# Performance work log

Measured on AMD Instinct MI355X. Metric: run time of the kernel, lower is better.

The kernel has to match this reference:

```python
import jax, jax.numpy as jnp
import numpy as np

K = 10          # top-k history news selected per candidate
THRESHOLD = 0.1 # attention-weight threshold (config.threshold)
EPS = 1e-12     # F.normalize eps


def setup_inputs() -> dict:
    key = jax.random.key(0)
    k1, k2, k3, k4 = jax.random.split(key, 4)
    B, C, H, L, LEV, D = 32, 5, 50, 32, 3, 256
    return {
        "cdd_repr": jax.random.normal(k1, (B, C, D), dtype=jnp.float32),
        "his_repr": jax.random.normal(k2, (B, H, D), dtype=jnp.float32),
        "his_embedding": jax.random.normal(k3, (B, H, L, LEV, D), dtype=jnp.float32),
        "W_sel": jax.random.normal(k4, (D, D), dtype=jnp.float32) * (1.0 / np.sqrt(D)),
        "b_sel": jnp.zeros((D,), dtype=jnp.float32),
    }


def _l2norm(x):
    # F.normalize(x, dim=-1): x / max(||x||, eps)
    n = jnp.sqrt(jnp.sum(x * x, axis=-1, keepdims=True))
    return x / jnp.maximum(n, EPS)


def reference(cdd_repr, his_repr, his_embedding, W_sel, b_sel):
    # selectionProject (Linear) + L2 normalize
    c = _l2norm(cdd_repr @ W_sel + b_sel)      # [B, C, D]
    h = _l2norm(his_repr @ W_sel + b_sel)      # [B, H, D]
    # news-level attention scores: cdd x his
    attn = jnp.einsum('bcd,bhd->bch', c, h)    # [B, C, H]
    # top-k over history
    w, idx = jax.lax.top_k(attn, K)            # [B, C, K]
    # gather selected history embeddings: [B, C, K, L, LEV, D]
    B = his_embedding.shape[0]
    his_activated = his_embedding[jnp.arange(B)[:, None, None], idx]
    # threshold masking then scale activated embeddings by attention weight
    w_masked = jnp.where(w < THRESHOLD, 0.0, w)
    his_activated = his_activated * w_masked[:, :, :, None, None, None]
    return his_activated
```

## Files before the change

kernel.cpp:

```cpp
#include <hip/hip_runtime.h>
#include <math.h>

#define BB 32
#define CC 5
#define HH 50
#define LL 32
#define LEV 3
#define DD 256
#define KK 10
#define THRESH 0.1f
#define EPSF 1e-12f
#define RPB 4
#define NPROJ ((BB * CC + BB * HH) / RPB)
#define INNER (LL * LEV * DD)
#define INNER4 (INNER / 4)
#define CHUNKS 4
#define PERCH (INNER4 / CHUNKS)

typedef float f32x4 __attribute__((ext_vector_type(4)));

__global__ void proj_norm_kernel(const float* __restrict__ cdd,
                                 const float* __restrict__ his,
                                 const float* __restrict__ W,
                                 const float* __restrict__ bias,
                                 float* __restrict__ c_out,
                                 float* __restrict__ h_out)
{
    const int row0 = blockIdx.x * RPB;
    const int j    = threadIdx.x;
    const int wid  = j >> 6;
    const int lane = j & 63;

    __shared__ float xs[RPB][DD];
    #pragma unroll
    for (int r = 0; r < RPB; ++r) {
        const int row = row0 + r;
        const float* x = (row < BB * CC) ? (cdd + (size_t)row * DD)
                                         : (his + (size_t)(row - BB * CC) * DD);
        xs[r][j] = x[j];
    }
    __syncthreads();

    const float bj = bias[j];
    float acc[RPB];
    #pragma unroll
    for (int r = 0; r < RPB; ++r) acc[r] = bj;

    for (int d = 0; d < DD; d += 4) {
        const float w0 = W[(size_t)(d + 0) * DD + j];
        const float w1 = W[(size_t)(d + 1) * DD + j];
        const float w2 = W[(size_t)(d + 2) * DD + j];
        const float w3 = W[(size_t)(d + 3) * DD + j];
        #pragma unroll
        for (int r = 0; r < RPB; ++r) {
            const float4 xv = *(const float4*)&xs[r][d];
            acc[r] = fmaf(xv.x, w0, fmaf(xv.y, w1, fmaf(xv.z, w2, fmaf(xv.w, w3, acc[r]))));
        }
    }

    __shared__ float part[RPB][4];
    #pragma unroll
    for (int r = 0; r < RPB; ++r) {
        float s = acc[r] * acc[r];
        #pragma unroll
        for (int off = 32; off > 0; off >>= 1) s += __shfl_xor(s, off, 64);
        if (lane == 0) part[r][wid] = s;
    }
    __syncthreads();
    __shared__ float inv_s[RPB];
    if (j < RPB) {
        const float s = part[j][0] + part[j][1] + part[j][2] + part[j][3];
        inv_s[j] = 1.0f / fmaxf(sqrtf(s), EPSF);
    }
    __syncthreads();

    #pragma unroll
    for (int r = 0; r < RPB; ++r) {
        const int row = row0 + r;
        float* y = (row < BB * CC) ? (c_out + (size_t)row * DD)
                                   : (h_out + (size_t)(row - BB * CC) * DD);
        y[j] = acc[r] * inv_s[r];
    }
}

__global__ void attn_topk_kernel(const float* __restrict__ c_n,
                                 const float* __restrict__ h_n,
                                 float2* __restrict__ wvidx)
{
    const int bc   = blockIdx.x;
    const int b    = bc / CC;
    const int tid  = threadIdx.x;
    const int wid  = tid >> 6;
    const int lane = tid & 63;

    __shared__ float cs[DD];
    __shared__ float attn_s[64];
    cs[tid] = c_n[(size_t)bc * DD + tid];
    if (tid < 64) attn_s[tid] = -INFINITY;
    __syncthreads();

    for (int h = wid; h < HH; h += 4) {
        const float* hr = h_n + (size_t)(b * HH + h) * DD;
        float p = 0.f;
        #pragma unroll
        for (int i = 0; i < 4; ++i) p += cs[lane + i * 64] * hr[lane + i * 64];
        #pragma unroll
        for (int off = 32; off > 0; off >>= 1) p += __shfl_down(p, off, 64);
        if (lane == 0) attn_s[h] = p;
    }
    __syncthreads();

    if (wid == 0) {
        float v   = attn_s[lane];
        int   myi = lane;
        for (int k = 0; k < KK; ++k) {
            float bv = v;
            int   bi = myi;
            #pragma unroll
            for (int off = 32; off > 0; off >>= 1) {
                const float ov = __shfl_xor(bv, off, 64);
                const int   oi = __shfl_xor(bi, off, 64);
                if (ov > bv || (ov == bv && oi < bi)) { bv = ov; bi = oi; }
            }
            if (lane == 0)
                wvidx[bc * KK + k] = make_float2((bv < THRESH) ? 0.0f : bv,
                                                 __int_as_float(bi));
            if (myi == bi) v = -INFINITY;
        }
    }
}

__global__ __launch_bounds__(256)
void gather_scale_kernel(const float* __restrict__ emb,
                         const float2* __restrict__ wvidx,
                         float* __restrict__ out)
{
    const int g     = blockIdx.x;
    const int blk   = g >> 2;
    const int chunk = g & 3;
    const int b     = blk / (CC * KK);

    const float2 wi = wvidx[blk];
    const float  w_ = wi.x;

    f32x4* dst = (f32x4*)(out + (size_t)blk * INNER) + chunk * PERCH + threadIdx.x;

    if (w_ == 0.0f) {
        const f32x4 z = (f32x4){0.f, 0.f, 0.f, 0.f};
        #pragma unroll
        for (int u = 0; u < PERCH / 256; ++u)
            __builtin_nontemporal_store(z, dst + 256 * u);
    } else {
        const int hi = __float_as_int(wi.y);
        const f32x4* src = (const f32x4*)(emb + (size_t)(b * HH + hi) * INNER)
                           + chunk * PERCH + threadIdx.x;
        f32x4 v[PERCH / 256];
        #pragma unroll
        for (int u = 0; u < PERCH / 256; ++u)
            v[u] = src[256 * u];
        #pragma unroll
        for (int u = 0; u < PERCH / 256; ++u)
            __builtin_nontemporal_store(v[u] * w_, dst + 256 * u);
    }
}

extern "C" void kernel_launch(void* const* d_in, const int* in_sizes, int n_in,
                              void* d_out, int out_size, void* d_ws, size_t ws_size,
                              hipStream_t stream) {
    const float* cdd  = (const float*)d_in[0];
    const float* his  = (const float*)d_in[1];
    const float* emb  = (const float*)d_in[2];
    const float* W    = (const float*)d_in[3];
    const float* bias = (const float*)d_in[4];
    float* out = (float*)d_out;

    char* ws = (char*)d_ws;
    float*  c_n   = (float*)ws;
    float*  h_n   = (float*)(ws + 163840);
    float2* wvidx = (float2*)(ws + 163840 + 1638400);

    proj_norm_kernel<<<NPROJ, DD, 0, stream>>>(cdd, his, W, bias, c_n, h_n);
    attn_topk_kernel<<<BB * CC, DD, 0, stream>>>(c_n, h_n, wvidx);
    gather_scale_kernel<<<BB * CC * KK * CHUNKS, 256, 0, stream>>>(emb, wvidx, out);
}
```

Measured before the change: 93.34 us.

## Replace per-row gather blocks with grid-stride flat gather and double projection rows

The gather/scale kernel becomes a persistent grid-stride loop over the whole flattened output with a fixed 2048 blocks. Each block first copies the full weight/index table into shared memory. Each element is then processed with a per-element index division and a branch, instead of a fixed 4-chunk block per selected row. The projection kernel now handles 8 rows per block instead of 4, which halves how often W is re-read. In exchange, each element pays an integer divide and each block loads the 1600-entry table, and each thread now has only one load in flight per iteration instead of several unrolled ones.

```diff
diff --git a/kernel.cpp b/kernel.cpp
--- a/kernel.cpp
+++ b/kernel.cpp
@@ -10,12 +10,13 @@
 #define KK 10
 #define THRESH 0.1f
 #define EPSF 1e-12f
-#define RPB 4
+#define RPB 8
 #define NPROJ ((BB * CC + BB * HH) / RPB)
 #define INNER (LL * LEV * DD)
 #define INNER4 (INNER / 4)
-#define CHUNKS 4
-#define PERCH (INNER4 / CHUNKS)
+#define NBCK (BB * CC * KK)
+#define TOTAL4 (NBCK * INNER4)
+#define NGBLK 2048
 
 typedef float f32x4 __attribute__((ext_vector_type(4)));
 
@@ -131,36 +132,32 @@
 }
 
 __global__ __launch_bounds__(256)
-void gather_scale_kernel(const float* __restrict__ emb,
-                         const float2* __restrict__ wvidx,
-                         float* __restrict__ out)
+void gather_flat_kernel(const float* __restrict__ emb,
+                        const float2* __restrict__ wvidx,
+                        float* __restrict__ out)
 {
-    const int g     = blockIdx.x;
-    const int blk   = g >> 2;
-    const int chunk = g & 3;
-    const int b     = blk / (CC * KK);
+    __shared__ float2 tbl[NBCK];
+    for (int t = threadIdx.x; t < NBCK; t += 256)
+        tbl[t] = wvidx[t];
+    __syncthreads();
 
-    const float2 wi = wvidx[blk];
-    const float  w_ = wi.x;
+    const f32x4* __restrict__ src4 = (const f32x4*)emb;
+    f32x4* __restrict__ dst4       = (f32x4*)out;
 
-    f32x4* dst = (f32x4*)(out + (size_t)blk * INNER) + chunk * PERCH + threadIdx.x;
+    const unsigned stride = NGBLK * 256;
+    for (unsigned i = blockIdx.x * 256 + threadIdx.x; i < TOTAL4; i += stride) {
+        const unsigned blk = i / INNER4;
+        const unsigned o4  = i - blk * INNER4;
+        const float2   wi  = tbl[blk];
 
-    if (w_ == 0.0f) {
-        const f32x4 z = (f32x4){0.f, 0.f, 0.f, 0.f};
-        #pragma unroll
-        for (int u = 0; u < PERCH / 256; ++u)
-            __builtin_nontemporal_store(z, dst + 256 * u);
-    } else {
-        const int hi = __float_as_int(wi.y);
-        const f32x4* src = (const f32x4*)(emb + (size_t)(b * HH + hi) * INNER)
-                           + chunk * PERCH + threadIdx.x;
-        f32x4 v[PERCH / 256];
-        #pragma unroll
-        for (int u = 0; u < PERCH / 256; ++u)
-            v[u] = src[256 * u];
-        #pragma unroll
-        for (int u = 0; u < PERCH / 256; ++u)
-            __builtin_nontemporal_store(v[u] * w_, dst + 256 * u);
+        if (wi.x == 0.0f) {
+            __builtin_nontemporal_store((f32x4){0.f, 0.f, 0.f, 0.f}, dst4 + i);
+        } else {
+            const unsigned b  = blk / (CC * KK);
+            const unsigned hi = __float_as_uint(wi.y);
+            const f32x4 v = src4[(size_t)(b * HH + hi) * INNER4 + o4];
+            __builtin_nontemporal_store(v * wi.x, dst4 + i);
+        }
     }
 }
 
@@ -181,5 +178,5 @@
 
     proj_norm_kernel<<<NPROJ, DD, 0, stream>>>(cdd, his, W, bias, c_n, h_n);
     attn_topk_kernel<<<BB * CC, DD, 0, stream>>>(c_n, h_n, wvidx);
-    gather_scale_kernel<<<BB * CC * KK * CHUNKS, 256, 0, stream>>>(emb, wvidx, out);
+    gather_flat_kernel<<<NGBLK, 256, 0, stream>>>(emb, wvidx, out);
 }
```

New measurement: 81.49 us. 1.15x faster.
